# Optimization experiments

Measured on AMD Instinct MI355X. Metric: run time of the kernel, lower is better.

The kernel has to match this reference:

```python
import jax, jax.numpy as jnp
import numpy as np

NUM_EMBEDDINGS = 8192
EMBEDDING_DIM = 512
COMMITMENT_COST = 0.25


def setup_inputs() -> dict:
    key = jax.random.key(0)
    kx, ke = jax.random.split(key)
    x = jax.random.normal(kx, (32, 512, 512), dtype=jnp.float32)
    # codebook ~ uniform init as in nn.Embedding default-ish; scale is arbitrary for a reference
    codebook = jax.random.normal(ke, (NUM_EMBEDDINGS, EMBEDDING_DIM), dtype=jnp.float32)
    return {"x": x, "codebook": codebook}


def reference(x, codebook):
    # x: [B, T, D], codebook: [K, D]
    input_shape = x.shape
    flat = x.reshape(-1, EMBEDDING_DIM)                     # [N, D]
    x2 = jnp.sum(flat * flat, axis=1, keepdims=True)        # [N, 1]
    e2 = jnp.sum(codebook * codebook, axis=1)               # [K]
    dists = x2 + e2 - 2.0 * jnp.matmul(flat, codebook.T)    # [N, K]
    encoding_indices = jnp.argmin(dists, axis=1)            # [N] int
    min_distances = jnp.min(dists, axis=1)                  # [N]
    quantized = codebook[encoding_indices].reshape(input_shape)  # [B, T, D]
    # straight-through estimator
    quantized_st = x + jax.lax.stop_gradient(quantized - x)
    # losses (sum reduction, matching F.mse_loss(..., reduction='sum'))
    loss_vq = jnp.sum((quantized - jax.lax.stop_gradient(x)) ** 2)
    loss_commit = jnp.sum((x - jax.lax.stop_gradient(quantized)) ** 2)
    # use_ema = False -> loss includes codebook term
    loss = loss_commit * COMMITMENT_COST + loss_vq
    encoding_indices = encoding_indices.reshape(input_shape[:-1])
    min_distances = min_distances.reshape(input_shape[:-1])
    return quantized_st, loss, encoding_indices, min_distances, loss_commit
```

## Files before the change

kernel.cpp:

```cpp
#include <hip/hip_runtime.h>
#include <hip/hip_bf16.h>
#include <math.h>

#define NUM_EMB 8192
#define DIM 512
#define NROWS 16384
#define NPART 4096

typedef unsigned short ushort;
typedef unsigned long long ull;
typedef __attribute__((ext_vector_type(8))) short short8;
typedef __attribute__((ext_vector_type(4))) float floatx4;

__device__ __forceinline__ ushort f2bf(float f) {
    unsigned u = __float_as_uint(f);
    unsigned r = (u + 0x7fffu + ((u >> 16) & 1u)) >> 16;
    return (ushort)r;
}
__device__ __forceinline__ float bf2f(ushort h) {
    return __uint_as_float(((unsigned)h) << 16);
}
__device__ __forceinline__ unsigned fmap(float f) {
    unsigned u = __float_as_uint(f);
    return (u & 0x80000000u) ? ~u : (u | 0x80000000u);
}
__device__ __forceinline__ float funmap(unsigned m) {
    return __uint_as_float((m & 0x80000000u) ? (m ^ 0x80000000u) : ~m);
}
__device__ __forceinline__ void gld16(const void* g, void* l) {
    __builtin_amdgcn_global_load_lds(
        (const __attribute__((address_space(1))) void*)g,
        (__attribute__((address_space(3))) void*)l, 16, 0, 0);
}

__global__ __launch_bounds__(256) void split_rss_k(const float* __restrict__ src,
    ushort* __restrict__ hi, ushort* __restrict__ lo, float* __restrict__ ss,
    ull* __restrict__ packed, int nrows)
{
    int gid  = blockIdx.x * blockDim.x + threadIdx.x;
    int row  = gid >> 6;
    int lane = threadIdx.x & 63;
    if (row >= nrows) return;
    const float4* r = (const float4*)(src + (size_t)row * DIM);
    ushort4* h4 = (ushort4*)(hi + (size_t)row * DIM);
    ushort4* l4 = (ushort4*)(lo + (size_t)row * DIM);
    float s = 0.f;
#pragma unroll
    for (int i = lane; i < DIM / 4; i += 64) {
        float4 v = r[i];
        s += v.x * v.x + v.y * v.y + v.z * v.z + v.w * v.w;
        ushort4 h, l;
        h.x = f2bf(v.x); l.x = f2bf(v.x - bf2f(h.x));
        h.y = f2bf(v.y); l.y = f2bf(v.y - bf2f(h.y));
        h.z = f2bf(v.z); l.z = f2bf(v.z - bf2f(h.z));
        h.w = f2bf(v.w); l.w = f2bf(v.w - bf2f(h.w));
        h4[i] = h; l4[i] = l;
    }
#pragma unroll
    for (int off = 32; off > 0; off >>= 1) s += __shfl_down(s, off, 64);
    if (lane == 0) {
        ss[row] = s;
        if (packed) packed[row] = ~0ull;
    }
}

__global__ __launch_bounds__(256, 4) void dist_mfma_k(
    const ushort* __restrict__ xh, const ushort* __restrict__ xl,
    const ushort* __restrict__ ch, const ushort* __restrict__ cl,
    const float* __restrict__ e2, ull* __restrict__ packed)
{
    __shared__ ushort Ah[128 * 32];
    __shared__ ushort Al[128 * 32];
    __shared__ ushort Bh[128 * 32];
    __shared__ ushort Bl[128 * 32];

    const int tid  = threadIdx.x;
    const int lane = tid & 63;
    const int w    = tid >> 6;
    const int wm   = w >> 1, wn = w & 1;
    const int row0 = blockIdx.x * 128;
    const int col0 = blockIdx.y * 128;

    floatx4 acc[4][4];
#pragma unroll
    for (int m = 0; m < 4; ++m)
#pragma unroll
        for (int n = 0; n < 4; ++n) acc[m][n] = (floatx4){0.f, 0.f, 0.f, 0.f};

    const int c0 = tid, c1 = tid + 256;
    const int r0c = c0 >> 2, s0c = (((c0 & 3) ^ ((c0 >> 3) & 3))) * 8;
    const int r1c = c1 >> 2, s1c = (((c1 & 3) ^ ((c1 >> 3) & 3))) * 8;
    const int ga0 = (row0 + r0c) * DIM + s0c;
    const int ga1 = (row0 + r1c) * DIM + s1c;
    const int gb0 = (col0 + r0c) * DIM + s0c;
    const int gb1 = (col0 + r1c) * DIM + s1c;
    const int l0 = c0 * 8, l1 = c1 * 8;

    const int fr = (lane & 15) * 32 + (((lane >> 4) ^ ((lane >> 1) & 3)) * 8);

    for (int kk = 0; kk < 16; ++kk) {
        const int dk = kk * 32;
        __syncthreads();
        gld16(&xh[ga0 + dk], &Ah[l0]);  gld16(&xh[ga1 + dk], &Ah[l1]);
        gld16(&xl[ga0 + dk], &Al[l0]);  gld16(&xl[ga1 + dk], &Al[l1]);
        gld16(&ch[gb0 + dk], &Bh[l0]);  gld16(&ch[gb1 + dk], &Bh[l1]);
        gld16(&cl[gb0 + dk], &Bl[l0]);  gld16(&cl[gb1 + dk], &Bl[l1]);
        __syncthreads();

        short8 ah[4], al[4], bh[4], bl[4];
#pragma unroll
        for (int m = 0; m < 4; ++m) {
            const int o = (wm * 64 + m * 16) * 32 + fr;
            ah[m] = *(const short8*)&Ah[o];
            al[m] = *(const short8*)&Al[o];
        }
#pragma unroll
        for (int n = 0; n < 4; ++n) {
            const int o = (wn * 64 + n * 16) * 32 + fr;
            bh[n] = *(const short8*)&Bh[o];
            bl[n] = *(const short8*)&Bl[o];
        }
#pragma unroll
        for (int m = 0; m < 4; ++m)
#pragma unroll
            for (int n = 0; n < 4; ++n) {
                acc[m][n] = __builtin_amdgcn_mfma_f32_16x16x32_bf16(ah[m], bh[n], acc[m][n], 0, 0, 0);
                acc[m][n] = __builtin_amdgcn_mfma_f32_16x16x32_bf16(ah[m], bl[n], acc[m][n], 0, 0, 0);
                acc[m][n] = __builtin_amdgcn_mfma_f32_16x16x32_bf16(al[m], bh[n], acc[m][n], 0, 0, 0);
            }
    }

    float e2v[4];
    int   cidx[4];
#pragma unroll
    for (int n = 0; n < 4; ++n) {
        cidx[n] = col0 + wn * 64 + n * 16 + (lane & 15);
        e2v[n]  = e2[cidx[n]];
    }
#pragma unroll
    for (int m = 0; m < 4; ++m) {
#pragma unroll
        for (int r = 0; r < 4; ++r) {
            float bv = INFINITY; int bi = 0x7fffffff;
#pragma unroll
            for (int n = 0; n < 4; ++n) {
                float v = e2v[n] - 2.f * acc[m][n][r];
                if (v < bv) { bv = v; bi = cidx[n]; }
            }
#pragma unroll
            for (int mk = 1; mk < 16; mk <<= 1) {
                float ov = __shfl_xor(bv, mk, 64);
                int   oi = __shfl_xor(bi, mk, 64);
                if (ov < bv || (ov == bv && oi < bi)) { bv = ov; bi = oi; }
            }
            if ((lane & 15) == 0) {
                int grow = row0 + wm * 64 + m * 16 + (lane >> 4) * 4 + r;
                ull pack = ((ull)fmap(bv) << 32) | (unsigned)bi;
                atomicMin(&packed[grow], pack);
            }
        }
    }
}

__global__ __launch_bounds__(256) void gather_loss_k(const float* __restrict__ x,
    const float* __restrict__ cb, const ull* __restrict__ packed,
    const float* __restrict__ x2, float* __restrict__ outq,
    float* __restrict__ out_idx, float* __restrict__ out_mind,
    float* __restrict__ partials)
{
    __shared__ float ps[4];
    int gid  = blockIdx.x * blockDim.x + threadIdx.x;
    int row  = gid >> 6;
    int lane = threadIdx.x & 63;
    int w    = threadIdx.x >> 6;
    float s = 0.f;
    if (row < NROWS) {
        ull p = packed[row];
        int k = (int)(p & 0xffffffffull);
        if (lane == 0) {
            out_idx[row]  = (float)k;
            out_mind[row] = x2[row] + funmap((unsigned)(p >> 32));
        }
        const float4* q  = (const float4*)(cb + (size_t)k * DIM);
        const float4* xr = (const float4*)(x + (size_t)row * DIM);
        float4* o = (float4*)(outq + (size_t)row * DIM);
#pragma unroll
        for (int i = lane; i < DIM / 4; i += 64) {
            float4 qv = q[i], xv = xr[i];
            o[i] = qv;
            float dx = xv.x - qv.x, dy = xv.y - qv.y;
            float dz = xv.z - qv.z, dw = xv.w - qv.w;
            s += dx * dx + dy * dy + dz * dz + dw * dw;
        }
    }
#pragma unroll
    for (int off = 32; off > 0; off >>= 1) s += __shfl_down(s, off, 64);
    if (lane == 0) ps[w] = s;
    __syncthreads();
    if (threadIdx.x == 0) partials[blockIdx.x] = ps[0] + ps[1] + ps[2] + ps[3];
}

__global__ __launch_bounds__(256) void finalize_k(const float* __restrict__ partials,
    float* __restrict__ out_loss, float* __restrict__ out_commit)
{
    __shared__ float ps[4];
    int t = threadIdx.x, lane = t & 63, w = t >> 6;
    float s = 0.f;
#pragma unroll
    for (int i = 0; i < NPART / 256; ++i) s += partials[t + 256 * i];
#pragma unroll
    for (int off = 32; off > 0; off >>= 1) s += __shfl_down(s, off, 64);
    if (lane == 0) ps[w] = s;
    __syncthreads();
    if (t == 0) {
        float tot = ps[0] + ps[1] + ps[2] + ps[3];
        *out_loss   = 0.25f * tot + tot;
        *out_commit = tot;
    }
}

#define BM 64
#define BN 64
#define BK 32
#define KSPLIT 4
#define KPER (NUM_EMB / KSPLIT)
#define NCT (KPER / BN)

__global__ __launch_bounds__(256) void rowsumsq_k(const float* __restrict__ a,
                                                  float* __restrict__ out, int nrows)
{
    int gid  = blockIdx.x * blockDim.x + threadIdx.x;
    int row  = gid >> 6;
    int lane = threadIdx.x & 63;
    if (row >= nrows) return;
    const float4* r = (const float4*)(a + (size_t)row * DIM);
    float s = 0.f;
#pragma unroll
    for (int i = lane; i < DIM / 4; i += 64) {
        float4 v = r[i];
        s += v.x * v.x + v.y * v.y + v.z * v.z + v.w * v.w;
    }
#pragma unroll
    for (int off = 32; off > 0; off >>= 1) s += __shfl_down(s, off, 64);
    if (lane == 0) out[row] = s;
}

__global__ __launch_bounds__(256) void dist_argmin_old_k(const float* __restrict__ x,
    const float* __restrict__ cb, const float* __restrict__ e2,
    float* __restrict__ part_m, int* __restrict__ part_i)
{
    __shared__ __align__(16) float As[BK][BM + 4];
    __shared__ __align__(16) float Bs[BK][BN + 4];
    __shared__ float redv[BM][16];
    __shared__ int   redi[BM][16];

    const int row0 = blockIdx.x * BM;
    const int ks   = blockIdx.y;
    const int cbeg = ks * KPER;
    const int t    = threadIdx.x;
    const int tx   = t & 15;
    const int ty   = t >> 4;
    const int ld_d = t & 31;
    const int ld_r = t >> 5;

    float minm[4]; int mini[4];
#pragma unroll
    for (int i = 0; i < 4; ++i) { minm[i] = INFINITY; mini[i] = 0; }

    for (int ct = 0; ct < NCT; ++ct) {
        const int c0 = cbeg + ct * BN;
        float acc[4][4];
#pragma unroll
        for (int i = 0; i < 4; ++i)
#pragma unroll
            for (int j = 0; j < 4; ++j) acc[i][j] = 0.f;
        for (int dc = 0; dc < DIM; dc += BK) {
#pragma unroll
            for (int rr = 0; rr < BM; rr += 8)
                As[ld_d][ld_r + rr] = x[(size_t)(row0 + ld_r + rr) * DIM + dc + ld_d];
#pragma unroll
            for (int rr = 0; rr < BN; rr += 8)
                Bs[ld_d][ld_r + rr] = cb[(size_t)(c0 + ld_r + rr) * DIM + dc + ld_d];
            __syncthreads();
#pragma unroll
            for (int d = 0; d < BK; ++d) {
                float4 av = *(const float4*)&As[d][4 * ty];
                float4 bv = *(const float4*)&Bs[d][4 * tx];
                acc[0][0] += av.x * bv.x; acc[0][1] += av.x * bv.y;
                acc[0][2] += av.x * bv.z; acc[0][3] += av.x * bv.w;
                acc[1][0] += av.y * bv.x; acc[1][1] += av.y * bv.y;
                acc[1][2] += av.y * bv.z; acc[1][3] += av.y * bv.w;
                acc[2][0] += av.z * bv.x; acc[2][1] += av.z * bv.y;
                acc[2][2] += av.z * bv.z; acc[2][3] += av.z * bv.w;
                acc[3][0] += av.w * bv.x; acc[3][1] += av.w * bv.y;
                acc[3][2] += av.w * bv.z; acc[3][3] += av.w * bv.w;
            }
            __syncthreads();
        }
#pragma unroll
        for (int j = 0; j < 4; ++j) {
            const int c = c0 + 4 * tx + j;
            const float e = e2[c];
#pragma unroll
            for (int i = 0; i < 4; ++i) {
                float m = e - 2.f * acc[i][j];
                if (m < minm[i]) { minm[i] = m; mini[i] = c; }
            }
        }
    }
#pragma unroll
    for (int i = 0; i < 4; ++i) {
        redv[4 * ty + i][tx] = minm[i];
        redi[4 * ty + i][tx] = mini[i];
    }
    __syncthreads();
    if (t < BM) {
        float bm = INFINITY; int bi = 0;
#pragma unroll
        for (int c = 0; c < 16; ++c) {
            float v = redv[t][c];
            if (v < bm) { bm = v; bi = redi[t][c]; }
        }
        part_m[(size_t)(row0 + t) * KSPLIT + ks] = bm;
        part_i[(size_t)(row0 + t) * KSPLIT + ks] = bi;
    }
}

__global__ __launch_bounds__(256) void merge_pack_k(const float* __restrict__ part_m,
    const int* __restrict__ part_i, ull* __restrict__ packed)
{
    int row = blockIdx.x * blockDim.x + threadIdx.x;
    if (row >= NROWS) return;
    float bm = INFINITY; int bi = 0;
#pragma unroll
    for (int s = 0; s < KSPLIT; ++s) {
        float v = part_m[(size_t)row * KSPLIT + s];
        if (v < bm) { bm = v; bi = part_i[(size_t)row * KSPLIT + s]; }
    }
    packed[row] = ((ull)fmap(bm) << 32) | (unsigned)bi;
}

extern "C" void kernel_launch(void* const* d_in, const int* in_sizes, int n_in,
                              void* d_out, int out_size, void* d_ws, size_t ws_size,
                              hipStream_t stream)
{
    const float* x  = (const float*)d_in[0];
    const float* cb = (const float*)d_in[1];
    float* out = (float*)d_out;

    float* outq       = out;
    float* out_loss   = out + 8388608;
    float* out_idx    = out + 8388609;
    float* out_mind   = out + 8388609 + 16384;
    float* out_commit = out + 8388609 + 2 * 16384;

    char* ws = (char*)d_ws;
    float* e2      = (float*)ws;   ws += NUM_EMB * 4;
    float* x2      = (float*)ws;   ws += NROWS * 4;
    ull*   packed  = (ull*)ws;     ws += NROWS * 8;
    float* partials= (float*)ws;   ws += NPART * 4;
    ushort* xh = (ushort*)ws;      ws += (size_t)NROWS * DIM * 2;
    ushort* xl = (ushort*)ws;      ws += (size_t)NROWS * DIM * 2;
    ushort* ch = (ushort*)ws;      ws += (size_t)NUM_EMB * DIM * 2;
    ushort* cl = (ushort*)ws;      ws += (size_t)NUM_EMB * DIM * 2;
    size_t need_fast = (size_t)(ws - (char*)d_ws);

    if (ws_size >= need_fast) {
        split_rss_k<<<NROWS / 4, 256, 0, stream>>>(x, xh, xl, x2, packed, NROWS);
        split_rss_k<<<NUM_EMB / 4, 256, 0, stream>>>(cb, ch, cl, e2, (ull*)0, NUM_EMB);
        dim3 grid(NROWS / 128, NUM_EMB / 128);
        dist_mfma_k<<<grid, 256, 0, stream>>>(xh, xl, ch, cl, e2, packed);
    } else {
        rowsumsq_k<<<NUM_EMB / 4, 256, 0, stream>>>(cb, e2, NUM_EMB);
        rowsumsq_k<<<NROWS / 4, 256, 0, stream>>>(x, x2, NROWS);
        float* pm = (float*)((char*)d_ws + NUM_EMB * 4 + NROWS * 4 + NROWS * 8 + NPART * 4);
        int*   pi = (int*)(pm + (size_t)NROWS * KSPLIT);
        dim3 grid(NROWS / BM, KSPLIT);
        dist_argmin_old_k<<<grid, 256, 0, stream>>>(x, cb, e2, pm, pi);
        merge_pack_k<<<NROWS / 256, 256, 0, stream>>>(pm, pi, packed);
    }

    gather_loss_k<<<NROWS / 4, 256, 0, stream>>>(x, cb, packed, x2, outq,
                                                 out_idx, out_mind, partials);
    finalize_k<<<1, 256, 0, stream>>>(partials, out_loss, out_commit);
}
```

Measured before the change: 486.1 us.

## Enlarge distance GEMM tile to 256x256 with double-buffered LDS staging

```diff
diff --git a/kernel.cpp b/kernel.cpp
--- a/kernel.cpp
+++ b/kernel.cpp
@@ -64,32 +64,32 @@
     }
 }
 
-__global__ __launch_bounds__(256, 4) void dist_mfma_k(
+__global__ __launch_bounds__(512, 2) void dist_mfma_k(
     const ushort* __restrict__ xh, const ushort* __restrict__ xl,
     const ushort* __restrict__ ch, const ushort* __restrict__ cl,
     const float* __restrict__ e2, ull* __restrict__ packed)
 {
-    __shared__ ushort Ah[128 * 32];
-    __shared__ ushort Al[128 * 32];
-    __shared__ ushort Bh[128 * 32];
-    __shared__ ushort Bl[128 * 32];
+    __shared__ ushort Ah[2][256 * 32];
+    __shared__ ushort Al[2][256 * 32];
+    __shared__ ushort Bh[2][256 * 32];
+    __shared__ ushort Bl[2][256 * 32];
 
     const int tid  = threadIdx.x;
     const int lane = tid & 63;
     const int w    = tid >> 6;
-    const int wm   = w >> 1, wn = w & 1;
-    const int row0 = blockIdx.x * 128;
-    const int col0 = blockIdx.y * 128;
-
-    floatx4 acc[4][4];
-#pragma unroll
-    for (int m = 0; m < 4; ++m)
+    const int wm   = w >> 2, wn = w & 3;
+    const int row0 = blockIdx.x * 256;
+    const int col0 = blockIdx.y * 256;
+
+    floatx4 acc[8][4];
+#pragma unroll
+    for (int m = 0; m < 8; ++m)
 #pragma unroll
         for (int n = 0; n < 4; ++n) acc[m][n] = (floatx4){0.f, 0.f, 0.f, 0.f};
 
-    const int c0 = tid, c1 = tid + 256;
-    const int r0c = c0 >> 2, s0c = (((c0 & 3) ^ ((c0 >> 3) & 3))) * 8;
-    const int r1c = c1 >> 2, s1c = (((c1 & 3) ^ ((c1 >> 3) & 3))) * 8;
+    const int c0 = tid, c1 = tid + 512;
+    const int r0c = c0 >> 2, s0c = ((c0 & 3) ^ ((c0 >> 3) & 3)) * 8;
+    const int r1c = c1 >> 2, s1c = ((c1 & 3) ^ ((c1 >> 3) & 3)) * 8;
     const int ga0 = (row0 + r0c) * DIM + s0c;
     const int ga1 = (row0 + r1c) * DIM + s1c;
     const int gb0 = (col0 + r0c) * DIM + s0c;
@@ -98,37 +98,46 @@
 
     const int fr = (lane & 15) * 32 + (((lane >> 4) ^ ((lane >> 1) & 3)) * 8);
 
-    for (int kk = 0; kk < 16; ++kk) {
+    auto stage = [&](int B, int kk) {
         const int dk = kk * 32;
-        __syncthreads();
-        gld16(&xh[ga0 + dk], &Ah[l0]);  gld16(&xh[ga1 + dk], &Ah[l1]);
-        gld16(&xl[ga0 + dk], &Al[l0]);  gld16(&xl[ga1 + dk], &Al[l1]);
-        gld16(&ch[gb0 + dk], &Bh[l0]);  gld16(&ch[gb1 + dk], &Bh[l1]);
-        gld16(&cl[gb0 + dk], &Bl[l0]);  gld16(&cl[gb1 + dk], &Bl[l1]);
-        __syncthreads();
-
-        short8 ah[4], al[4], bh[4], bl[4];
-#pragma unroll
-        for (int m = 0; m < 4; ++m) {
-            const int o = (wm * 64 + m * 16) * 32 + fr;
-            ah[m] = *(const short8*)&Ah[o];
-            al[m] = *(const short8*)&Al[o];
-        }
+        gld16(&xh[ga0 + dk], &Ah[B][l0]);  gld16(&xh[ga1 + dk], &Ah[B][l1]);
+        gld16(&xl[ga0 + dk], &Al[B][l0]);  gld16(&xl[ga1 + dk], &Al[B][l1]);
+        gld16(&ch[gb0 + dk], &Bh[B][l0]);  gld16(&ch[gb1 + dk], &Bh[B][l1]);
+        gld16(&cl[gb0 + dk], &Bl[B][l0]);  gld16(&cl[gb1 + dk], &Bl[B][l1]);
+    };
+    auto compute = [&](int B) {
+        short8 bh[4], bl[4];
 #pragma unroll
         for (int n = 0; n < 4; ++n) {
             const int o = (wn * 64 + n * 16) * 32 + fr;
-            bh[n] = *(const short8*)&Bh[o];
-            bl[n] = *(const short8*)&Bl[o];
-        }
-#pragma unroll
-        for (int m = 0; m < 4; ++m)
+            bh[n] = *(const short8*)&Bh[B][o];
+            bl[n] = *(const short8*)&Bl[B][o];
+        }
+#pragma unroll
+        for (int m = 0; m < 8; ++m) {
+            const int o = (wm * 128 + m * 16) * 32 + fr;
+            short8 ah = *(const short8*)&Ah[B][o];
+            short8 al = *(const short8*)&Al[B][o];
 #pragma unroll
             for (int n = 0; n < 4; ++n) {
-                acc[m][n] = __builtin_amdgcn_mfma_f32_16x16x32_bf16(ah[m], bh[n], acc[m][n], 0, 0, 0);
-                acc[m][n] = __builtin_amdgcn_mfma_f32_16x16x32_bf16(ah[m], bl[n], acc[m][n], 0, 0, 0);
-                acc[m][n] = __builtin_amdgcn_mfma_f32_16x16x32_bf16(al[m], bh[n], acc[m][n], 0, 0, 0);
-            }
-    }
+                acc[m][n] = __builtin_amdgcn_mfma_f32_16x16x32_bf16(ah, bh[n], acc[m][n], 0, 0, 0);
+                acc[m][n] = __builtin_amdgcn_mfma_f32_16x16x32_bf16(ah, bl[n], acc[m][n], 0, 0, 0);
+                acc[m][n] = __builtin_amdgcn_mfma_f32_16x16x32_bf16(al, bh[n], acc[m][n], 0, 0, 0);
+            }
+        }
+    };
+
+    stage(0, 0);
+    __syncthreads();
+    int cur = 0;
+#pragma unroll 1
+    for (int kk = 0; kk < 15; ++kk) {
+        stage(cur ^ 1, kk + 1);
+        compute(cur);
+        __syncthreads();
+        cur ^= 1;
+    }
+    compute(cur);
 
     float e2v[4];
     int   cidx[4];
@@ -138,7 +147,7 @@
         e2v[n]  = e2[cidx[n]];
     }
 #pragma unroll
-    for (int m = 0; m < 4; ++m) {
+    for (int m = 0; m < 8; ++m) {
 #pragma unroll
         for (int r = 0; r < 4; ++r) {
             float bv = INFINITY; int bi = 0x7fffffff;
@@ -154,7 +163,7 @@
                 if (ov < bv || (ov == bv && oi < bi)) { bv = ov; bi = oi; }
             }
             if ((lane & 15) == 0) {
-                int grow = row0 + wm * 64 + m * 16 + (lane >> 4) * 4 + r;
+                int grow = row0 + wm * 128 + m * 16 + (lane >> 4) * 4 + r;
                 ull pack = ((ull)fmap(bv) << 32) | (unsigned)bi;
                 atomicMin(&packed[grow], pack);
             }
@@ -368,8 +377,8 @@
     if (ws_size >= need_fast) {
         split_rss_k<<<NROWS / 4, 256, 0, stream>>>(x, xh, xl, x2, packed, NROWS);
         split_rss_k<<<NUM_EMB / 4, 256, 0, stream>>>(cb, ch, cl, e2, (ull*)0, NUM_EMB);
-        dim3 grid(NROWS / 128, NUM_EMB / 128);
-        dist_mfma_k<<<grid, 256, 0, stream>>>(xh, xl, ch, cl, e2, packed);
+        dim3 grid(NROWS / 256, NUM_EMB / 256);
+        dist_mfma_k<<<grid, 512, 0, stream>>>(xh, xl, ch, cl, e2, packed);
     } else {
         rowsumsq_k<<<NUM_EMB / 4, 256, 0, stream>>>(cb, e2, NUM_EMB);
         rowsumsq_k<<<NROWS / 4, 256, 0, stream>>>(x, x2, NROWS);
```

Result: slower. 529.2 us (+8.9%).
